# Kernel tuning notes

Measured on AMD Instinct MI355X. Metric: run time of the kernel, lower is better.

Reference implementation:

```python
import jax, jax.numpy as jnp
import numpy as np

D_MODEL = 1024
N_HEADS = 16
D_K = D_MODEL // N_HEADS
SEQ = 4096
BATCH = 1
THETA = 10000.0


def setup_inputs() -> dict:
    key = jax.random.key(0)
    ks = jax.random.split(key, 5)
    scale = 0.02
    x = jax.random.normal(ks[0], (BATCH, SEQ, D_MODEL), dtype=jnp.float32)
    token_positions = jnp.broadcast_to(jnp.arange(SEQ, dtype=jnp.int64 if jax.config.jax_enable_x64 else jnp.int32)[None, :], (BATCH, SEQ))
    Wq = jax.random.normal(ks[1], (D_MODEL, D_MODEL), dtype=jnp.float32) * scale
    Wk = jax.random.normal(ks[2], (D_MODEL, D_MODEL), dtype=jnp.float32) * scale
    Wv = jax.random.normal(ks[3], (D_MODEL, D_MODEL), dtype=jnp.float32) * scale
    Wo = jax.random.normal(ks[4], (D_MODEL, D_MODEL), dtype=jnp.float32) * scale
    return {"x": x, "token_positions": token_positions, "Wq": Wq, "Wk": Wk, "Wv": Wv, "Wo": Wo}


def _apply_rope(t, token_positions, theta=THETA):
    # t: (b, h, s, d_k); token_positions: (b, s)
    d_k = t.shape[-1]
    inv_freq = theta ** (-jnp.arange(0, d_k, 2, dtype=jnp.float32) / d_k)  # (d_k/2,)
    ang = token_positions.astype(jnp.float32)[:, :, None] * inv_freq  # (b, s, d_k/2)
    cos = jnp.cos(ang)[:, None, :, :]  # (b, 1, s, d_k/2)
    sin = jnp.sin(ang)[:, None, :, :]
    te, to = t[..., 0::2], t[..., 1::2]
    re = te * cos - to * sin
    ro = te * sin + to * cos
    # interleave back: (..., d_k/2, 2) -> (..., d_k)
    return jnp.stack([re, ro], axis=-1).reshape(t.shape)


def reference(x, token_positions, Wq, Wk, Wv, Wo):
    b, s, d_model = x.shape
    h, d_k = N_HEADS, D_K
    q = (x @ Wq.T).reshape(b, s, h, d_k).transpose(0, 2, 1, 3)  # (b,h,s,d_k)
    k = (x @ Wk.T).reshape(b, s, h, d_k).transpose(0, 2, 1, 3)
    v = (x @ Wv.T).reshape(b, s, h, d_k).transpose(0, 2, 1, 3)
    q = _apply_rope(q, token_positions)
    k = _apply_rope(k, token_positions)
    scores = jnp.einsum('bhqd,bhkd->bhqk', q, k) / jnp.sqrt(jnp.float32(d_k))
    causal = jnp.tril(jnp.ones((s, s), dtype=bool))[None, None]
    scores = jnp.where(causal, scores, jnp.float32(-1e9))
    attn = jax.nn.softmax(scores, axis=-1)
    out = jnp.einsum('bhqk,bhkd->bhqd', attn, v)  # (b,h,s,d_k)
    out = out.transpose(0, 2, 1, 3).reshape(b, s, d_model)
    return out @ Wo.T
```

## Files before the change

kernel.cpp:

```cpp
#include <hip/hip_runtime.h>
#include <hip/hip_bf16.h>
#include <math.h>


#define SEQ 4096
#define DM  1024
#define NH  16
#define DK  64

typedef __attribute__((ext_vector_type(8))) short short8;
typedef __attribute__((ext_vector_type(4))) float floatx4;
typedef __attribute__((ext_vector_type(4))) short short4v;

static __device__ __forceinline__ short f2bf(float f) {
    __hip_bfloat16 h = __float2bfloat16(f);
    return __builtin_bit_cast(short, h);
}

static __device__ __forceinline__ float fast_exp2(float x) {
#if __has_builtin(__builtin_amdgcn_exp2f)
    return __builtin_amdgcn_exp2f(x);
#else
    return exp2f(x);
#endif
}

static __device__ __forceinline__ short8 load8_f32_as_bf16(const float* p) {
    float4 a = *reinterpret_cast<const float4*>(p);
    float4 b = *reinterpret_cast<const float4*>(p + 4);
    short8 s;
    s[0] = f2bf(a.x); s[1] = f2bf(a.y); s[2] = f2bf(a.z); s[3] = f2bf(a.w);
    s[4] = f2bf(b.x); s[5] = f2bf(b.y); s[6] = f2bf(b.z); s[7] = f2bf(b.w);
    return s;
}

static __device__ __forceinline__ void gl2lds16(const __hip_bfloat16* g, short* l) {
    __builtin_amdgcn_global_load_lds(
        (const __attribute__((address_space(1))) unsigned int*)g,
        (__attribute__((address_space(3))) unsigned int*)l, 16, 0, 0);
}

static __device__ __forceinline__ int read_pos(const int* tp32, int s) {
    return (tp32[1] == 1) ? tp32[s] : tp32[2 * s];
}

__global__ __launch_bounds__(256) void prep_kernel(
    const float* __restrict__ x,  const float* __restrict__ Wq,
    const float* __restrict__ Wk, const float* __restrict__ Wv,
    const int* __restrict__ tp,
    __hip_bfloat16* __restrict__ xb,  __hip_bfloat16* __restrict__ Wqb,
    __hip_bfloat16* __restrict__ Wkb, __hip_bfloat16* __restrict__ Wvb,
    float2* __restrict__ tab)
{
    int b = blockIdx.x;
    if (b < 3584) {
        const float* src; __hip_bfloat16* dst; int off;
        if (b < 2048)      { src = x;  dst = xb;  off = b; }
        else if (b < 2560) { src = Wq; dst = Wqb; off = b - 2048; }
        else if (b < 3072) { src = Wk; dst = Wkb; off = b - 2560; }
        else               { src = Wv; dst = Wvb; off = b - 3072; }
        size_t i = (size_t)off * 256 + threadIdx.x;
        short8 v = load8_f32_as_bf16(src + i * 8);
        *reinterpret_cast<short8*>((short*)dst + i * 8) = v;
    } else {
        int idx = (b - 3584) * 256 + threadIdx.x;
        if (idx < SEQ * 32) {
            int s = idx >> 5, pair = idx & 31;
            float inv_freq = exp2f(-(float)(2 * pair) * (13.287712379549449f / 64.f));
            float sn, cs;
            sincosf((float)read_pos(tp, s) * inv_freq, &sn, &cs);
            tab[idx] = make_float2(cs, sn);
        }
    }
}

__global__ __launch_bounds__(256) void qkv_rope_kernel(
    const __hip_bfloat16* __restrict__ xb,
    const float2* __restrict__ tab,
    const __hip_bfloat16* __restrict__ Wqb,
    const __hip_bfloat16* __restrict__ Wkb,
    const __hip_bfloat16* __restrict__ Wvb,
    __hip_bfloat16* __restrict__ q_ws,
    __hip_bfloat16* __restrict__ k_ws,
    __hip_bfloat16* __restrict__ vt_ws)
{
    __shared__ __align__(16) short pool[17408];
    short* As = pool;
    short* Bs = pool + 8192;

    const int by = blockIdx.y;
    const int wsel = by >> 3;
    const __hip_bfloat16* W = (wsel == 0) ? Wqb : (wsel == 1 ? Wkb : Wvb);
    const int nloc0 = (by & 7) * 128;
    const int m0 = blockIdx.x * 128;

    const int t = threadIdx.x;
    const int lane = t & 63;
    const int w = t >> 6;
    const int quad = lane >> 4;
    const int ln = lane & 15;
    const int wm = (w >> 1) * 64;
    const int wn = (w & 1) * 64;

    floatx4 acc[4][4];
    #pragma unroll
    for (int i = 0; i < 4; i++)
        #pragma unroll
        for (int j = 0; j < 4; j++) acc[i][j] = (floatx4){0.f, 0.f, 0.f, 0.f};

    for (int k0 = 0; k0 < DM; k0 += 64) {
        #pragma unroll
        for (int it = 0; it < 4; it++) {
            int row = w * 32 + it * 8 + (lane >> 3);
            int sg = (lane & 7) ^ (row & 7);
            gl2lds16(&xb[(size_t)(m0 + row) * DM + k0 + sg * 8], &As[(w * 32 + it * 8) * 64]);
            gl2lds16(&W[(size_t)(nloc0 + row) * DM + k0 + sg * 8], &Bs[(w * 32 + it * 8) * 64]);
        }
        __syncthreads();

        short8 af[4][2], bfr[4][2];
        #pragma unroll
        for (int i = 0; i < 4; i++)
            #pragma unroll
            for (int kc = 0; kc < 2; kc++)
                af[i][kc] = *reinterpret_cast<const short8*>(
                    &As[(wm + i * 16 + ln) * 64 + (((kc * 4 + quad) ^ (ln & 7)) << 3)]);
        #pragma unroll
        for (int j = 0; j < 4; j++)
            #pragma unroll
            for (int kc = 0; kc < 2; kc++)
                bfr[j][kc] = *reinterpret_cast<const short8*>(
                    &Bs[(wn + j * 16 + ln) * 64 + (((kc * 4 + quad) ^ (ln & 7)) << 3)]);

        #pragma unroll
        for (int kc = 0; kc < 2; kc++)
            #pragma unroll
            for (int i = 0; i < 4; i++)
                #pragma unroll
                for (int j = 0; j < 4; j++)
                    acc[i][j] = __builtin_amdgcn_mfma_f32_16x16x32_bf16(
                        af[i][kc], bfr[j][kc], acc[i][j], 0, 0, 0);
        __syncthreads();
    }

    if (wsel < 2) {
        __hip_bfloat16* dst = (wsel == 0) ? q_ws : k_ws;
        const float qscale = (wsel == 0) ? 0.18033688011112042f : 1.0f;
        #pragma unroll
        for (int j = 0; j < 4; j++) {
            int cnl = wn + j * 16 + ln;
            int pair = ((nloc0 + cnl) & 63) >> 1;
            #pragma unroll
            for (int i = 0; i < 4; i++) {
                int rowl = wm + i * 16 + quad * 4;
                #pragma unroll
                for (int r = 0; r < 4; r++) {
                    float2 t2 = tab[(size_t)(m0 + rowl + r) * 32 + pair];
                    float val = acc[i][j][r];
                    float partner = __shfl_xor(val, 1, 64);
                    float res = val * t2.x + (((lane & 1) ? partner : -partner) * t2.y);
                    pool[(rowl + r) * 136 + cnl] = f2bf(res * qscale);
                }
            }
        }
        __syncthreads();
        int row = t >> 1, half = t & 1;
        size_t gbase = (size_t)(m0 + row) * DM + nloc0 + half * 64;
        #pragma unroll
        for (int c = 0; c < 8; c++)
            *reinterpret_cast<short8*>(&dst[gbase + c * 8]) =
                *reinterpret_cast<const short8*>(&pool[row * 136 + half * 64 + c * 8]);
    } else {
        #pragma unroll
        for (int j = 0; j < 4; j++) {
            int cnl = wn + j * 16 + ln;
            #pragma unroll
            for (int i = 0; i < 4; i++) {
                int s0 = wm + i * 16 + quad * 4;
                #pragma unroll
                for (int r = 0; r < 4; r++)
                    pool[cnl * 136 + s0 + r] = f2bf(acc[i][j][r]);
            }
        }
        __syncthreads();
        int cnl = t >> 1, sh = t & 1;
        size_t base = (size_t)(nloc0 + cnl) * SEQ + m0 + sh * 64;
        #pragma unroll
        for (int c = 0; c < 8; c++)
            *reinterpret_cast<short8*>(&vt_ws[base + c * 8]) =
                *reinterpret_cast<const short8*>(&pool[cnl * 136 + sh * 64 + c * 8]);
    }
}

__global__ __launch_bounds__(256, 2) void attn_kernel(
    const __hip_bfloat16* __restrict__ q_ws,
    const __hip_bfloat16* __restrict__ k_ws,
    const __hip_bfloat16* __restrict__ vt_ws,
    __hip_bfloat16* __restrict__ o_ws)
{
    __shared__ __align__(16) short Kt[2][2][64 * 64];
    __shared__ __align__(16) short Vt[2][2][64 * 64];
    __shared__ __align__(16) short P[4][2][16 * 64];

    const int bid = (int)blockIdx.x + 32 * (int)blockIdx.y;
    const int wg  = (bid & 7) * 64 + (bid >> 3);
    const int head = wg >> 5;
    const int bx   = wg & 31;

    const int qbA0 = (63 - bx) * 64;
    const int qbB0 = bx * 64;
    const int t = threadIdx.x;
    const int lane = t & 63;
    const int w = t >> 6;
    const int quad = lane >> 4;
    const int ln = lane & 15;
    const int nstep = (qbA0 + 63) / 128 + 1;

    const int qAbase = qbA0 + w * 16;
    const int qBbase = qbB0 + w * 16;
    const int e = ((ln & 7) << 1) ^ (ln & 8);

    auto stage = [&](int b, int kb) {
        #pragma unroll
        for (int h = 0; h < 2; h++)
            #pragma unroll
            for (int i = 0; i < 2; i++) {
                int keyl = w * 16 + i * 8 + (lane >> 3);
                int sg = (lane & 7) ^ (keyl & 7);
                gl2lds16(&k_ws[(size_t)(kb + h * 64 + keyl) * DM + head * 64 + sg * 8],
                         &Kt[b][h][(w * 16 + i * 8) * 64]);
                gl2lds16(&vt_ws[(size_t)(head * 64 + keyl) * SEQ + kb + h * 64 + sg * 8],
                         &Vt[b][h][(w * 16 + i * 8) * 64]);
            }
    };

    short8 qfA[2], qfB[2];
    #pragma unroll
    for (int kk = 0; kk < 2; kk++) {
        qfA[kk] = *reinterpret_cast<const short8*>(
            &q_ws[(size_t)(qAbase + ln) * DM + head * 64 + kk * 32 + quad * 8]);
        qfB[kk] = *reinterpret_cast<const short8*>(
            &q_ws[(size_t)(qBbase + ln) * DM + head * 64 + kk * 32 + quad * 8]);
    }

    floatx4 accA[4], accB[4];
    float lA = 0.f, lB = 0.f;
    #pragma unroll
    for (int nt = 0; nt < 4; nt++) {
        accA[nt] = (floatx4){0.f, 0.f, 0.f, 0.f};
        accB[nt] = (floatx4){0.f, 0.f, 0.f, 0.f};
    }
    const floatx4 zero4 = {0.f, 0.f, 0.f, 0.f};

    stage(0, 0);
    int buf = 0;
    for (int st = 0; st < nstep; st++) {
        __syncthreads();
        if (st + 1 < nstep) stage(buf ^ 1, (st + 1) * 128);

        #pragma unroll
        for (int h = 0; h < 2; h++) {
            const int kb = st * 128 + h * 64;
            const bool actA = (h == 0) || (kb <= qAbase + 15);
            const bool actB = (kb <= qBbase + 15);
            if (!actA && !actB) continue;

            short8 kf[4][2], vf[4][2];
            #pragma unroll
            for (int nt = 0; nt < 4; nt++)
                #pragma unroll
                for (int kk = 0; kk < 2; kk++) {
                    const int off = (nt * 16 + ln) * 64 + (((kk * 4 + quad) ^ (ln & 7)) << 3);
                    kf[nt][kk] = *reinterpret_cast<const short8*>(&Kt[buf][h][off]);
                    vf[nt][kk] = *reinterpret_cast<const short8*>(&Vt[buf][h][off]);
                }

            auto qk_sm = [&](const short8 (&qf)[2], float& l, int qbase, int pslot) {
                floatx4 s[4];
                __builtin_amdgcn_s_setprio(1);
                #pragma unroll
                for (int nt = 0; nt < 4; nt++) {
                    floatx4 x0 = __builtin_amdgcn_mfma_f32_16x16x32_bf16(kf[nt][0], qf[0], zero4, 0, 0, 0);
                    s[nt] = __builtin_amdgcn_mfma_f32_16x16x32_bf16(kf[nt][1], qf[1], x0, 0, 0, 0);
                }
                __builtin_amdgcn_s_setprio(0);
                const int qpos = qbase + ln;
                if (kb + 63 > qbase) {
                    #pragma unroll
                    for (int nt = 0; nt < 4; nt++) {
                        int kbase = kb + nt * 16 + quad * 4;
                        #pragma unroll
                        for (int r = 0; r < 4; r++)
                            if (kbase + r > qpos) s[nt][r] = -1e9f;
                    }
                }
                #pragma unroll
                for (int nt = 0; nt < 4; nt++) {
                    #pragma unroll
                    for (int r = 0; r < 4; r++) {
                        float p = fast_exp2(s[nt][r]);
                        s[nt][r] = p;
                        l += p;
                    }
                    short4v pk = { f2bf(s[nt][0]), f2bf(s[nt][1]),
                                   f2bf(s[nt][2]), f2bf(s[nt][3]) };
                    *reinterpret_cast<short4v*>(&P[w][pslot][ln * 64 + (((nt * 4 + quad) ^ e) << 2)]) = pk;
                }
            };
            auto pv = [&](floatx4 (&acc)[4], int pslot) {
                short8 pa[2];
                #pragma unroll
                for (int kk = 0; kk < 2; kk++)
                    pa[kk] = *reinterpret_cast<const short8*>(
                        &P[w][pslot][ln * 64 + (((kk * 8 + quad * 2) ^ e) << 2)]);
                __builtin_amdgcn_s_setprio(1);
                #pragma unroll
                for (int nt = 0; nt < 4; nt++) {
                    floatx4 o = __builtin_amdgcn_mfma_f32_16x16x32_bf16(pa[0], vf[nt][0], acc[nt], 0, 0, 0);
                    acc[nt] = __builtin_amdgcn_mfma_f32_16x16x32_bf16(pa[1], vf[nt][1], o, 0, 0, 0);
                }
                __builtin_amdgcn_s_setprio(0);
            };

            if (actA) qk_sm(qfA, lA, qAbase, 0);
            if (actB) qk_sm(qfB, lB, qBbase, 1);
            if (actA) pv(accA, 0);
            if (actB) pv(accB, 1);
        }
        buf ^= 1;
    }

    {
        float l = lA;
        l += __shfl_xor(l, 16, 64);
        l += __shfl_xor(l, 32, 64);
        #pragma unroll
        for (int r = 0; r < 4; r++) {
            float rl = 1.f / __shfl(l, quad * 4 + r, 64);
            int row = qAbase + quad * 4 + r;
            #pragma unroll
            for (int nt = 0; nt < 4; nt++)
                o_ws[(size_t)row * DM + head * 64 + nt * 16 + ln] =
                    __float2bfloat16(accA[nt][r] * rl);
        }
    }
    {
        float l = lB;
        l += __shfl_xor(l, 16, 64);
        l += __shfl_xor(l, 32, 64);
        #pragma unroll
        for (int r = 0; r < 4; r++) {
            float rl = 1.f / __shfl(l, quad * 4 + r, 64);
            int row = qBbase + quad * 4 + r;
            #pragma unroll
            for (int nt = 0; nt < 4; nt++)
                o_ws[(size_t)row * DM + head * 64 + nt * 16 + ln] =
                    __float2bfloat16(accB[nt][r] * rl);
        }
    }
}

__global__ __launch_bounds__(256) void oproj_kernel(
    const __hip_bfloat16* __restrict__ o_in,
    const float* __restrict__ Wo,
    float* __restrict__ out)
{
    __shared__ __align__(16) char smem[24576];
    short* As = (short*)smem;
    short* Bs = As + 8192;
    float* fpool = (float*)smem;

    const int m0 = blockIdx.x * 128;
    const int n0 = blockIdx.y * 64;

    const int t = threadIdx.x;
    const int lane = t & 63;
    const int w = t >> 6;
    const int quad = lane >> 4;
    const int ln = lane & 15;
    const int wm = (w >> 1) * 64;
    const int wn = (w & 1) * 32;

    floatx4 acc[4][2];
    #pragma unroll
    for (int i = 0; i < 4; i++)
        #pragma unroll
        for (int j = 0; j < 2; j++) acc[i][j] = (floatx4){0.f, 0.f, 0.f, 0.f};

    for (int k0 = 0; k0 < DM; k0 += 64) {
        #pragma unroll
        for (int it = 0; it < 4; it++) {
            int row = w * 32 + it * 8 + (lane >> 3);
            int sg = (lane & 7) ^ (row & 7);
            gl2lds16(&o_in[(size_t)(m0 + row) * DM + k0 + sg * 8], &As[(w * 32 + it * 8) * 64]);
        }
        #pragma unroll
        for (int p = 0; p < 2; p++) {
            int r = (t >> 3) + p * 32;
            int sg2 = t & 7;
            *reinterpret_cast<short8*>(&Bs[r * 64 + ((sg2 ^ (r & 7)) << 3)]) =
                load8_f32_as_bf16(&Wo[(size_t)(n0 + r) * DM + k0 + sg2 * 8]);
        }
        __syncthreads();

        short8 af[4][2], bfr[2][2];
        #pragma unroll
        for (int i = 0; i < 4; i++)
            #pragma unroll
            for (int kc = 0; kc < 2; kc++)
                af[i][kc] = *reinterpret_cast<const short8*>(
                    &As[(wm + i * 16 + ln) * 64 + (((kc * 4 + quad) ^ (ln & 7)) << 3)]);
        #pragma unroll
        for (int j = 0; j < 2; j++)
            #pragma unroll
            for (int kc = 0; kc < 2; kc++)
                bfr[j][kc] = *reinterpret_cast<const short8*>(
                    &Bs[(wn + j * 16 + ln) * 64 + (((kc * 4 + quad) ^ (ln & 7)) << 3)]);

        #pragma unroll
        for (int kc = 0; kc < 2; kc++)
            #pragma unroll
            for (int i = 0; i < 4; i++)
                #pragma unroll
                for (int j = 0; j < 2; j++)
                    acc[i][j] = __builtin_amdgcn_mfma_f32_16x16x32_bf16(
                        af[i][kc], bfr[j][kc], acc[i][j], 0, 0, 0);
        __syncthreads();
    }

    #pragma unroll
    for (int ph = 0; ph < 2; ph++) {
        if ((w >> 1) == ph) {
            #pragma unroll
            for (int j = 0; j < 2; j++)
                #pragma unroll
                for (int i = 0; i < 4; i++) {
                    int rl = i * 16 + quad * 4;
                    #pragma unroll
                    for (int r = 0; r < 4; r++)
                        fpool[(rl + r) * 68 + wn + j * 16 + ln] = acc[i][j][r];
                }
        }
        __syncthreads();
        int row = t >> 2;
        int c0 = (t & 3) * 16;
        size_t gbase = (size_t)(m0 + ph * 64 + row) * DM + n0 + c0;
        #pragma unroll
        for (int c = 0; c < 4; c++)
            *reinterpret_cast<float4*>(&out[gbase + c * 4]) =
                *reinterpret_cast<const float4*>(&fpool[row * 68 + c0 + c * 4]);
        __syncthreads();
    }
}

extern "C" void kernel_launch(void* const* d_in, const int* in_sizes, int n_in,
                              void* d_out, int out_size, void* d_ws, size_t ws_size,
                              hipStream_t stream) {
    const float* x  = (const float*)d_in[0];
    const int* tp   = (const int*)d_in[1];
    const float* Wq = (const float*)d_in[2];
    const float* Wk = (const float*)d_in[3];
    const float* Wv = (const float*)d_in[4];
    const float* Wo = (const float*)d_in[5];
    float* out = (float*)d_out;

    char* ws = (char*)d_ws;
    const size_t MB = 1024 * 1024;
    __hip_bfloat16* xb    = (__hip_bfloat16*)(ws);
    __hip_bfloat16* q_ws  = (__hip_bfloat16*)(ws + 8  * MB);
    __hip_bfloat16* k_ws  = (__hip_bfloat16*)(ws + 16 * MB);
    __hip_bfloat16* vt_ws = (__hip_bfloat16*)(ws + 24 * MB);
    __hip_bfloat16* o_ws  = xb;
    __hip_bfloat16* Wqb = (__hip_bfloat16*)d_out;
    __hip_bfloat16* Wkb = Wqb + (size_t)DM * DM;
    __hip_bfloat16* Wvb = Wkb + (size_t)DM * DM;
    float2* tab = (float2*)((char*)d_out + 6 * MB);

    prep_kernel<<<4096, 256, 0, stream>>>(x, Wq, Wk, Wv, tp, xb, Wqb, Wkb, Wvb, tab);
    qkv_rope_kernel<<<dim3(32, 24), 256, 0, stream>>>(xb, tab, Wqb, Wkb, Wvb, q_ws, k_ws, vt_ws);
    attn_kernel<<<dim3(32, 16), 256, 0, stream>>>(q_ws, k_ws, vt_ws, o_ws);
    oproj_kernel<<<dim3(32, 16), 256, 0, stream>>>(o_ws, Wo, out);
}
```

Measured before the change: 218.1 us.

## Rewrite attention with 32x32x16 MFMA, register-resident P, and 128-row query tiles

The attention kernel moves from 16x16x32 MFMA with two paired query tiles per block to 32x32x16 MFMA, where each wave owns 32 query rows of a 128-row tile. The softmax probabilities stay in registers and feed the PV MFMA directly, so the P round-trip through LDS goes away. The grid becomes 512 blocks, ordered longest-first to balance the causal workload, and output is written through an LDS staging buffer as coalesced 16-byte stores. The price is higher register pressure from the 16-wide accumulators, which may lower occupancy, and the A/B tile pairing that previously balanced work inside each block is gone.

```diff
diff --git a/kernel.cpp b/kernel.cpp
--- a/kernel.cpp
+++ b/kernel.cpp
@@ -10,6 +10,7 @@
 
 typedef __attribute__((ext_vector_type(8))) short short8;
 typedef __attribute__((ext_vector_type(4))) float floatx4;
+typedef __attribute__((ext_vector_type(16))) float floatx16;
 typedef __attribute__((ext_vector_type(4))) short short4v;
 
 static __device__ __forceinline__ short f2bf(float f) {
@@ -198,164 +199,147 @@
     const __hip_bfloat16* __restrict__ vt_ws,
     __hip_bfloat16* __restrict__ o_ws)
 {
-    __shared__ __align__(16) short Kt[2][2][64 * 64];
-    __shared__ __align__(16) short Vt[2][2][64 * 64];
-    __shared__ __align__(16) short P[4][2][16 * 64];
-
-    const int bid = (int)blockIdx.x + 32 * (int)blockIdx.y;
-    const int wg  = (bid & 7) * 64 + (bid >> 3);
-    const int head = wg >> 5;
-    const int bx   = wg & 31;
-
-    const int qbA0 = (63 - bx) * 64;
-    const int qbB0 = bx * 64;
+    __shared__ __align__(16) short Kt[2][128 * 64];
+    __shared__ __align__(16) short Vt[2][64 * 128];
+
+    const int bid = (int)blockIdx.x;
+    const int head = bid & 15;
+    const int tile = (bid < 256) ? (31 - (bid >> 4)) : ((bid - 256) >> 4);
+    const int nstep = tile + 1;
+
     const int t = threadIdx.x;
     const int lane = t & 63;
     const int w = t >> 6;
-    const int quad = lane >> 4;
-    const int ln = lane & 15;
-    const int nstep = (qbA0 + 63) / 128 + 1;
-
-    const int qAbase = qbA0 + w * 16;
-    const int qBbase = qbB0 + w * 16;
-    const int e = ((ln & 7) << 1) ^ (ln & 8);
+    const int hi = lane >> 5;
+    const int l31 = lane & 31;
+    const int q0 = tile * 128 + w * 32;
 
     auto stage = [&](int b, int kb) {
         #pragma unroll
-        for (int h = 0; h < 2; h++)
-            #pragma unroll
-            for (int i = 0; i < 2; i++) {
-                int keyl = w * 16 + i * 8 + (lane >> 3);
-                int sg = (lane & 7) ^ (keyl & 7);
-                gl2lds16(&k_ws[(size_t)(kb + h * 64 + keyl) * DM + head * 64 + sg * 8],
-                         &Kt[b][h][(w * 16 + i * 8) * 64]);
-                gl2lds16(&vt_ws[(size_t)(head * 64 + keyl) * SEQ + kb + h * 64 + sg * 8],
-                         &Vt[b][h][(w * 16 + i * 8) * 64]);
-            }
+        for (int i = 0; i < 4; i++) {
+            int r = w * 32 + i * 8 + (lane >> 3);
+            int keyloc = (r & ~12) | ((r & 4) << 1) | ((r & 8) >> 1);
+            int g = (lane & 7) ^ (r & 7);
+            gl2lds16(&k_ws[(size_t)(kb + keyloc) * DM + head * 64 + g * 8],
+                     &Kt[b][(w * 32 + i * 8) * 64]);
+        }
+        #pragma unroll
+        for (int i = 0; i < 4; i++) {
+            int d = w * 16 + i * 4 + (lane >> 4);
+            int g = (lane & 15) ^ (d & 7);
+            gl2lds16(&vt_ws[(size_t)(head * 64 + d) * SEQ + kb + g * 8],
+                     &Vt[b][(w * 16 + i * 4) * 128]);
+        }
     };
 
-    short8 qfA[2], qfB[2];
-    #pragma unroll
-    for (int kk = 0; kk < 2; kk++) {
-        qfA[kk] = *reinterpret_cast<const short8*>(
-            &q_ws[(size_t)(qAbase + ln) * DM + head * 64 + kk * 32 + quad * 8]);
-        qfB[kk] = *reinterpret_cast<const short8*>(
-            &q_ws[(size_t)(qBbase + ln) * DM + head * 64 + kk * 32 + quad * 8]);
-    }
-
-    floatx4 accA[4], accB[4];
-    float lA = 0.f, lB = 0.f;
-    #pragma unroll
-    for (int nt = 0; nt < 4; nt++) {
-        accA[nt] = (floatx4){0.f, 0.f, 0.f, 0.f};
-        accB[nt] = (floatx4){0.f, 0.f, 0.f, 0.f};
-    }
-    const floatx4 zero4 = {0.f, 0.f, 0.f, 0.f};
+    short8 qf[4];
+    #pragma unroll
+    for (int c = 0; c < 4; c++)
+        qf[c] = *reinterpret_cast<const short8*>(
+            &q_ws[(size_t)(q0 + l31) * DM + head * 64 + c * 16 + hi * 8]);
+
+    floatx16 accO[2];
+    #pragma unroll
+    for (int db = 0; db < 2; db++)
+        #pragma unroll
+        for (int i = 0; i < 16; i++) accO[db][i] = 0.f;
+    float l = 0.f;
 
     stage(0, 0);
     int buf = 0;
     for (int st = 0; st < nstep; st++) {
         __syncthreads();
         if (st + 1 < nstep) stage(buf ^ 1, (st + 1) * 128);
-
-        #pragma unroll
-        for (int h = 0; h < 2; h++) {
-            const int kb = st * 128 + h * 64;
-            const bool actA = (h == 0) || (kb <= qAbase + 15);
-            const bool actB = (kb <= qBbase + 15);
-            if (!actA && !actB) continue;
-
-            short8 kf[4][2], vf[4][2];
-            #pragma unroll
-            for (int nt = 0; nt < 4; nt++)
-                #pragma unroll
-                for (int kk = 0; kk < 2; kk++) {
-                    const int off = (nt * 16 + ln) * 64 + (((kk * 4 + quad) ^ (ln & 7)) << 3);
-                    kf[nt][kk] = *reinterpret_cast<const short8*>(&Kt[buf][h][off]);
-                    vf[nt][kk] = *reinterpret_cast<const short8*>(&Vt[buf][h][off]);
+        const bool last = (st == nstep - 1);
+
+        #pragma unroll
+        for (int kb32 = 0; kb32 < 4; kb32++) {
+            if (!(last && kb32 > w)) {
+                const int krow = kb32 * 32 + l31;
+                short8 kfr[4];
+                #pragma unroll
+                for (int kc = 0; kc < 4; kc++) {
+                    int g = (kc * 2 + hi) ^ (krow & 7);
+                    kfr[kc] = *reinterpret_cast<const short8*>(&Kt[buf][krow * 64 + g * 8]);
                 }
-
-            auto qk_sm = [&](const short8 (&qf)[2], float& l, int qbase, int pslot) {
-                floatx4 s[4];
+                floatx16 s;
+                #pragma unroll
+                for (int i = 0; i < 16; i++) s[i] = 0.f;
                 __builtin_amdgcn_s_setprio(1);
                 #pragma unroll
-                for (int nt = 0; nt < 4; nt++) {
-                    floatx4 x0 = __builtin_amdgcn_mfma_f32_16x16x32_bf16(kf[nt][0], qf[0], zero4, 0, 0, 0);
-                    s[nt] = __builtin_amdgcn_mfma_f32_16x16x32_bf16(kf[nt][1], qf[1], x0, 0, 0, 0);
-                }
+                for (int kc = 0; kc < 4; kc++)
+                    s = __builtin_amdgcn_mfma_f32_32x32x16_bf16(kfr[kc], qf[kc], s, 0, 0, 0);
                 __builtin_amdgcn_s_setprio(0);
-                const int qpos = qbase + ln;
-                if (kb + 63 > qbase) {
+
+                if (last) {
                     #pragma unroll
-                    for (int nt = 0; nt < 4; nt++) {
-                        int kbase = kb + nt * 16 + quad * 4;
-                        #pragma unroll
-                        for (int r = 0; r < 4; r++)
-                            if (kbase + r > qpos) s[nt][r] = -1e9f;
+                    for (int r = 0; r < 16; r++) {
+                        int key_l = kb32 * 32 + (r & 7) + 2 * (r & 8) + 8 * hi;
+                        if (key_l > w * 32 + l31) s[r] = -1e9f;
                     }
                 }
-                #pragma unroll
-                for (int nt = 0; nt < 4; nt++) {
+                float p[16];
+                #pragma unroll
+                for (int r = 0; r < 16; r++) { p[r] = fast_exp2(s[r]); l += p[r]; }
+
+                union { short8 v; short e[8]; } pb[2];
+                #pragma unroll
+                for (int c = 0; c < 2; c++)
                     #pragma unroll
-                    for (int r = 0; r < 4; r++) {
-                        float p = fast_exp2(s[nt][r]);
-                        s[nt][r] = p;
-                        l += p;
+                    for (int e8 = 0; e8 < 8; e8++)
+                        pb[c].e[e8] = f2bf(p[c * 8 + e8]);
+
+                #pragma unroll
+                for (int db = 0; db < 2; db++) {
+                    const int vrow = db * 32 + l31;
+                    short8 vfr[2];
+                    #pragma unroll
+                    for (int c = 0; c < 2; c++) {
+                        int g = (kb32 * 4 + c * 2 + hi) ^ (vrow & 7);
+                        vfr[c] = *reinterpret_cast<const short8*>(&Vt[buf][vrow * 128 + g * 8]);
                     }
-                    short4v pk = { f2bf(s[nt][0]), f2bf(s[nt][1]),
-                                   f2bf(s[nt][2]), f2bf(s[nt][3]) };
-                    *reinterpret_cast<short4v*>(&P[w][pslot][ln * 64 + (((nt * 4 + quad) ^ e) << 2)]) = pk;
+                    __builtin_amdgcn_s_setprio(1);
+                    accO[db] = __builtin_amdgcn_mfma_f32_32x32x16_bf16(vfr[0], pb[0].v, accO[db], 0, 0, 0);
+                    accO[db] = __builtin_amdgcn_mfma_f32_32x32x16_bf16(vfr[1], pb[1].v, accO[db], 0, 0, 0);
+                    __builtin_amdgcn_s_setprio(0);
                 }
-            };
-            auto pv = [&](floatx4 (&acc)[4], int pslot) {
-                short8 pa[2];
-                #pragma unroll
-                for (int kk = 0; kk < 2; kk++)
-                    pa[kk] = *reinterpret_cast<const short8*>(
-                        &P[w][pslot][ln * 64 + (((kk * 8 + quad * 2) ^ e) << 2)]);
-                __builtin_amdgcn_s_setprio(1);
-                #pragma unroll
-                for (int nt = 0; nt < 4; nt++) {
-                    floatx4 o = __builtin_amdgcn_mfma_f32_16x16x32_bf16(pa[0], vf[nt][0], acc[nt], 0, 0, 0);
-                    acc[nt] = __builtin_amdgcn_mfma_f32_16x16x32_bf16(pa[1], vf[nt][1], o, 0, 0, 0);
-                }
-                __builtin_amdgcn_s_setprio(0);
-            };
-
-            if (actA) qk_sm(qfA, lA, qAbase, 0);
-            if (actB) qk_sm(qfB, lB, qBbase, 1);
-            if (actA) pv(accA, 0);
-            if (actB) pv(accB, 1);
+            }
         }
         buf ^= 1;
     }
 
+    float lf = l + __shfl_xor(l, 32, 64);
+    float rl = 1.f / lf;
+
+    __syncthreads();
+    short* pool = (short*)Kt;
+    const int qrow = w * 32 + l31;
+    #pragma unroll
+    for (int db = 0; db < 2; db++)
+        #pragma unroll
+        for (int j = 0; j < 4; j++) {
+            union { short4v v; short e[4]; } g;
+            #pragma unroll
+            for (int m = 0; m < 4; m++)
+                g.e[m] = f2bf(accO[db][j * 4 + m] * rl);
+            int dcol = db * 32 + j * 8 + 4 * hi;
+            *reinterpret_cast<short4v*>(&pool[qrow * 68 + dcol]) = g.v;
+        }
+    __syncthreads();
+
     {
-        float l = lA;
-        l += __shfl_xor(l, 16, 64);
-        l += __shfl_xor(l, 32, 64);
-        #pragma unroll
-        for (int r = 0; r < 4; r++) {
-            float rl = 1.f / __shfl(l, quad * 4 + r, 64);
-            int row = qAbase + quad * 4 + r;
-            #pragma unroll
-            for (int nt = 0; nt < 4; nt++)
-                o_ws[(size_t)row * DM + head * 64 + nt * 16 + ln] =
-                    __float2bfloat16(accA[nt][r] * rl);
-        }
-    }
-    {
-        float l = lB;
-        l += __shfl_xor(l, 16, 64);
-        l += __shfl_xor(l, 32, 64);
-        #pragma unroll
-        for (int r = 0; r < 4; r++) {
-            float rl = 1.f / __shfl(l, quad * 4 + r, 64);
-            int row = qBbase + quad * 4 + r;
-            #pragma unroll
-            for (int nt = 0; nt < 4; nt++)
-                o_ws[(size_t)row * DM + head * 64 + nt * 16 + ln] =
-                    __float2bfloat16(accB[nt][r] * rl);
+        int r = t >> 1, hh = t & 1;
+        size_t gb = (size_t)(tile * 128 + r) * DM + head * 64 + hh * 32;
+        #pragma unroll
+        for (int c = 0; c < 2; c++) {
+            union { short8 v8; short4v h[2]; } u;
+            u.h[0] = *reinterpret_cast<const short4v*>(&pool[r * 68 + hh * 32 + c * 16]);
+            u.h[1] = *reinterpret_cast<const short4v*>(&pool[r * 68 + hh * 32 + c * 16 + 4]);
+            *reinterpret_cast<short8*>(&o_ws[gb + c * 16]) = u.v8;
+            union { short8 v8; short4v h[2]; } u2;
+            u2.h[0] = *reinterpret_cast<const short4v*>(&pool[r * 68 + hh * 32 + c * 16 + 8]);
+            u2.h[1] = *reinterpret_cast<const short4v*>(&pool[r * 68 + hh * 32 + c * 16 + 12]);
+            *reinterpret_cast<short8*>(&o_ws[gb + c * 16 + 8]) = u2.v8;
         }
     }
 }
@@ -478,6 +462,6 @@
 
     prep_kernel<<<4096, 256, 0, stream>>>(x, Wq, Wk, Wv, tp, xb, Wqb, Wkb, Wvb, tab);
     qkv_rope_kernel<<<dim3(32, 24), 256, 0, stream>>>(xb, tab, Wqb, Wkb, Wvb, q_ws, k_ws, vt_ws);
-    attn_kernel<<<dim3(32, 16), 256, 0, stream>>>(q_ws, k_ws, vt_ws, o_ws);
+    attn_kernel<<<512, 256, 0, stream>>>(q_ws, k_ws, vt_ws, o_ws);
     oproj_kernel<<<dim3(32, 16), 256, 0, stream>>>(o_ws, Wo, out);
 }
```

Result: no change. 220.1 us (+0.9%).
